# Kernel tuning notes

Measured on AMD Instinct MI355X. Metric: run time of the kernel, lower is better.

## Reference

```python
import jax, jax.numpy as jnp
import numpy as np

B = 2048      # env batch (graphs)
A = 8         # agents per graph (fully connected)
N = B * A     # total nodes
DIN = 192     # raw obs dim
HD = 256      # h_dim (base MLP)
MD = 256      # mem_dim (GRU)
GD = 128      # gnn_dim (per-head GATv2 out, concat=False -> head mean)
H = 4         # GAT heads
NA = 20       # n_actions
ED = 3        # edge_dim


def setup_inputs() -> dict:
    key = jax.random.key(0)
    ks = jax.random.split(key, 16)
    # fully-connected directed graph per group of A agents, no self loops
    s, d = np.meshgrid(np.arange(A), np.arange(A), indexing='ij')
    mask = s != d
    s = s[mask]; d = d[mask]                     # [A*(A-1)]
    off = (np.arange(B) * A)[:, None]
    src = (off + s[None, :]).reshape(-1)
    dst = (off + d[None, :]).reshape(-1)
    edge_index = jnp.asarray(np.stack([src, dst]), dtype=jnp.int32)  # [2, E]
    E = src.shape[0]
    p = lambda k, sh: jax.random.normal(ks[k], sh, jnp.float32) * 0.02
    return {
        'inputs': jax.random.normal(ks[0], (N, DIN), jnp.float32),
        'hidden_states': jax.random.normal(ks[1], (N, MD), jnp.float32) * 0.1,
        'edge_index': edge_index,
        'edge_attr': jax.random.uniform(ks[2], (E, ED), jnp.float32),
        # base MLP (2 layers: Linear+ReLU+LayerNorm)
        'W1': p(3, (DIN, HD)), 'b1': jnp.zeros(HD), 'g1': jnp.ones(HD), 'be1': jnp.zeros(HD),
        'W2': p(4, (HD, HD)),  'b2': jnp.zeros(HD), 'g2': jnp.ones(HD), 'be2': jnp.zeros(HD),
        # GRUCell
        'Wih': p(5, (3 * MD, HD)), 'Whh': p(6, (3 * MD, MD)),
        'bih': jnp.zeros(3 * MD), 'bhh': jnp.zeros(3 * MD),
        # GATv2Conv (edge_dim=3, heads=4, concat=False, residual)
        'Wl': p(7, (MD, H * GD)), 'bl': jnp.zeros(H * GD),
        'Wr': p(8, (MD, H * GD)), 'br': jnp.zeros(H * GD),
        'att': p(9, (H, GD)),
        'We': p(10, (ED, H * GD)),
        'Wres': p(11, (MD, GD)),
        'bg': jnp.zeros(GD),
        # head: LayerNorm + Linear
        'lng': jnp.ones(GD), 'lnb': jnp.zeros(GD),
        'Wout': p(12, (GD, NA)), 'bout': jnp.zeros(NA),
    }


def _ln(x, g, b):
    mu = jnp.mean(x, -1, keepdims=True)
    xc = x - mu
    v = jnp.mean(xc * xc, -1, keepdims=True)
    return xc * jax.lax.rsqrt(v + 1e-5) * g + b


def _fwd(inputs, hidden_states, edge_attr, edge_index,
         W1, b1, g1, be1, W2, b2, g2, be2,
         Wih, Whh, bih, bhh,
         Wl, bl, Wr, br, att, We, Wres, bg,
         lng, lnb, Wout, bout):
    src, dst = edge_index[0], edge_index[1]
    # ---- base MLP encode ----
    x = _ln(jax.nn.relu(inputs @ W1 + b1), g1, be1)
    x = _ln(jax.nn.relu(x @ W2 + b2), g2, be2)          # [N, HD]
    # ---- SimpleConv(aggr='mean', combine_root='self_loop') ----
    s = jax.ops.segment_sum(x[src], dst, num_segments=N) + x
    deg = jax.ops.segment_sum(jnp.ones(src.shape[0], x.dtype), dst, num_segments=N) + 1.0
    x = s / deg[:, None]                                 # [N, HD]
    # ---- GRUCell ----
    gi = x @ Wih.T + bih
    gh = hidden_states @ Whh.T + bhh
    ir, iz, inn = jnp.split(gi, 3, -1)
    hr, hz, hn = jnp.split(gh, 3, -1)
    r = jax.nn.sigmoid(ir + hr)
    z = jax.nn.sigmoid(iz + hz)
    n = jnp.tanh(inn + r * hn)
    h = (1.0 - z) * n + z * hidden_states                # [N, MD]
    # ---- GATv2Conv (add self loops, edge_attr fill='mean') ----
    loop = jnp.arange(N, dtype=src.dtype)
    sf = jnp.concatenate([src, loop])
    df = jnp.concatenate([dst, loop])
    ea = jnp.concatenate([edge_attr, jnp.broadcast_to(edge_attr.mean(0), (N, ED))], 0)
    xl = (h @ Wl + bl).reshape(N, H, GD)
    xr = (h @ Wr + br).reshape(N, H, GD)
    m = xl[sf] + xr[df] + (ea @ We).reshape(-1, H, GD)   # [Ef, H, GD]
    m = jnp.where(m > 0, m, 0.2 * m)                     # leaky_relu(0.2)
    logits = jnp.einsum('ehc,hc->eh', m, att)            # [Ef, H]
    mx = jax.ops.segment_max(logits, df, num_segments=N)
    ex = jnp.exp(logits - mx[df])
    den = jax.ops.segment_sum(ex, df, num_segments=N)
    alpha = ex / (den[df] + 1e-16)                       # segment softmax
    out = jax.ops.segment_sum(xl[sf] * alpha[..., None], df, num_segments=N)
    out = out.mean(1) + h @ Wres + bg                    # head mean + residual + bias
    zg = jax.nn.relu(out)                                # [N, GD]
    # ---- action head ----
    q = _ln(zg, lng, lnb) @ Wout + bout                  # [N, NA]
    return q, h


def reference(inputs, hidden_states, edge_index, edge_attr,
              W1, b1, g1, be1, W2, b2, g2, be2,
              Wih, Whh, bih, bhh,
              Wl, bl, Wr, br, att, We, Wres, bg,
              lng, lnb, Wout, bout):
    return _fwd(inputs, hidden_states, edge_attr, edge_index,
                W1, b1, g1, be1, W2, b2, g2, be2,
                Wih, Whh, bih, bhh,
                Wl, bl, Wr, br, att, We, Wres, bg,
                lng, lnb, Wout, bout)
```

## Files before the change

### kernel.cpp

```cpp
#include <hip/hip_runtime.h>
#include <hip/hip_bf16.h>

constexpr int NB  = 2048;
constexpr int AG  = 8;
constexpr int NN  = NB * AG;
constexpr int DIN = 192;
constexpr int HD  = 256;
constexpr int MD  = 256;
constexpr int GD  = 128;
constexpr int NA  = 20;
constexpr int NE  = NB * AG * (AG - 1);

typedef __attribute__((ext_vector_type(8))) short bfrag8;
typedef __attribute__((ext_vector_type(4))) short sfrag4;
typedef __attribute__((ext_vector_type(4))) float f32x4;

#define MFMA16(a, b, c) __builtin_amdgcn_mfma_f32_16x16x32_bf16((a), (b), (c), 0, 0, 0)

__device__ __forceinline__ float bf2f(__hip_bfloat16 x) { return __bfloat162float(x); }
__device__ __forceinline__ __hip_bfloat16 f2bf(float x) { return __float2bfloat16(x); }
__device__ __forceinline__ short f2bs(float x) {
    __hip_bfloat16 b = __float2bfloat16(x);
    return *reinterpret_cast<short*>(&b);
}
__device__ __forceinline__ bfrag8 ldf(const __hip_bfloat16* p) { return *(const bfrag8*)p; }
__device__ __forceinline__ bfrag8 ldf32(const float* p) {
    const f32x4 a = *(const f32x4*)p;
    const f32x4 b = *(const f32x4*)(p + 4);
    bfrag8 r;
    r[0] = f2bs(a[0]); r[1] = f2bs(a[1]); r[2] = f2bs(a[2]); r[3] = f2bs(a[3]);
    r[4] = f2bs(b[0]); r[5] = f2bs(b[1]); r[6] = f2bs(b[2]); r[7] = f2bs(b[3]);
    return r;
}
__device__ __forceinline__ float sigmf(float x) { return 1.f / (1.f + __expf(-x)); }
__device__ __forceinline__ float blo(unsigned u) { return __uint_as_float(u << 16); }
__device__ __forceinline__ float bhi(unsigned u) { return __uint_as_float(u & 0xffff0000u); }

__global__ __launch_bounds__(256) void k_prep(
    const float* __restrict__ W1, const float* __restrict__ W2,
    const float* __restrict__ Wih, const float* __restrict__ Whh,
    const float* __restrict__ Wl, const float* __restrict__ bl,
    const float* __restrict__ Wr, const float* __restrict__ br,
    const float* __restrict__ Wres, const float* __restrict__ Wout,
    __hip_bfloat16* __restrict__ W1T, __hip_bfloat16* __restrict__ W2T,
    __hip_bfloat16* __restrict__ WihB, __hip_bfloat16* __restrict__ WhhB,
    __hip_bfloat16* __restrict__ WcatT, float* __restrict__ WoutTf,
    float* __restrict__ bcat)
{
    int i = blockIdx.x * 256 + threadIdx.x;
    if (i < 49152) { int o = i / 192, c = i % 192; W1T[i] = f2bf(W1[c * 256 + o]); return; }
    i -= 49152;
    if (i < 65536) { int o = i >> 8, c = i & 255; W2T[i] = f2bf(W2[c * 256 + o]); return; }
    i -= 65536;
    if (i < 196608) { WihB[i] = f2bf(Wih[i]); return; }
    i -= 196608;
    if (i < 196608) { WhhB[i] = f2bf(Whh[i]); return; }
    i -= 196608;
    if (i < 294912) {
        int o = i >> 8, c = i & 255;
        float v;
        if (o < 512)       v = Wl[c * 512 + o];
        else if (o < 1024) v = Wr[c * 512 + (o - 512)];
        else               v = Wres[c * 128 + (o - 1024)];
        WcatT[i] = f2bf(v); return;
    }
    i -= 294912;
    if (i < 2560) { int o = i >> 7, c = i & 127; WoutTf[i] = Wout[c * 20 + o]; return; }
    i -= 2560;
    if (i < 1152) {
        float v = 0.f;
        if (i < 512) v = bl[i]; else if (i < 1024) v = br[i - 512];
        bcat[i] = v;
    }
}

__global__ __launch_bounds__(256) void k_easum1(const float* __restrict__ ea,
                                                float* __restrict__ partials)
{
    __shared__ float sw[4][3];
    const int b = blockIdx.x, tid = threadIdx.x;
    float a0 = 0.f, a1 = 0.f, a2 = 0.f;
#pragma unroll
    for (int k = 0; k < 7; k++) {
        int e = b * 1792 + k * 256 + tid;
        a0 += ea[e * 3 + 0];
        a1 += ea[e * 3 + 1];
        a2 += ea[e * 3 + 2];
    }
#pragma unroll
    for (int off = 1; off < 64; off <<= 1) {
        a0 += __shfl_xor(a0, off); a1 += __shfl_xor(a1, off); a2 += __shfl_xor(a2, off);
    }
    if ((tid & 63) == 0) { sw[tid >> 6][0] = a0; sw[tid >> 6][1] = a1; sw[tid >> 6][2] = a2; }
    __syncthreads();
    if (tid == 0) {
        partials[b * 3 + 0] = sw[0][0] + sw[1][0] + sw[2][0] + sw[3][0];
        partials[b * 3 + 1] = sw[0][1] + sw[1][1] + sw[2][1] + sw[3][1];
        partials[b * 3 + 2] = sw[0][2] + sw[1][2] + sw[2][2] + sw[3][2];
    }
}

__global__ void k_easum2(const float* __restrict__ partials, float* __restrict__ ea_mean)
{
    int t = threadIdx.x;
    if (t < 3) {
        float s = 0.f;
        for (int i = 0; i < 64; i++) s += partials[i * 3 + t];
        ea_mean[t] = s * (1.f / NE);
    }
}

__global__ __launch_bounds__(256) void k_encode(
    const float* __restrict__ in,
    const __hip_bfloat16* __restrict__ W1T,
    const float* __restrict__ b1, const float* __restrict__ g1, const float* __restrict__ be1,
    const __hip_bfloat16* __restrict__ W2T,
    const float* __restrict__ b2, const float* __restrict__ g2, const float* __restrict__ be2,
    __hip_bfloat16* __restrict__ xm)
{
    __shared__ float sf[16][257];
    __shared__ alignas(16) __hip_bfloat16 sb[16][264];
    const int tid = threadIdx.x;
    const int lane = tid & 63, w = tid >> 6;
    const int r = lane & 15, q = lane >> 4;
    const int m0 = blockIdx.x * 16;

    f32x4 acc[4];
#pragma unroll
    for (int i = 0; i < 4; i++) acc[i] = (f32x4){0.f, 0.f, 0.f, 0.f};

    {
        const float* ap = in + (size_t)(m0 + r) * DIN + q * 8;
#pragma unroll
        for (int kb = 0; kb < 6; kb++) {
            bfrag8 af = ldf32(ap + kb * 32);
#pragma unroll
            for (int i = 0; i < 4; i++) {
                int t = w * 4 + i;
                bfrag8 bfv = ldf(W1T + (size_t)(t * 16 + r) * DIN + kb * 32 + q * 8);
                acc[i] = MFMA16(af, bfv, acc[i]);
            }
        }
    }
#pragma unroll
    for (int i = 0; i < 4; i++) {
        int col = (w * 4 + i) * 16 + r;
        float bias = b1[col];
#pragma unroll
        for (int reg = 0; reg < 4; reg++)
            sf[q * 4 + reg][col] = fmaxf(acc[i][reg] + bias, 0.f);
    }
    __syncthreads();
    {
        int rowi = tid >> 4, c16 = tid & 15;
        float vals[16]; float s = 0.f, s2 = 0.f;
#pragma unroll
        for (int j = 0; j < 16; j++) { float v = sf[rowi][c16 + 16 * j]; vals[j] = v; s += v; s2 += v * v; }
#pragma unroll
        for (int off = 1; off < 16; off <<= 1) { s += __shfl_xor(s, off); s2 += __shfl_xor(s2, off); }
        float mean = s * (1.f / HD);
        float var = fmaxf(s2 * (1.f / HD) - mean * mean, 0.f);
        float rs = rsqrtf(var + 1e-5f);
#pragma unroll
        for (int j = 0; j < 16; j++) {
            int col = c16 + 16 * j;
            sb[rowi][col] = f2bf((vals[j] - mean) * rs * g1[col] + be1[col]);
        }
    }
    __syncthreads();

#pragma unroll
    for (int i = 0; i < 4; i++) acc[i] = (f32x4){0.f, 0.f, 0.f, 0.f};
    {
        const __hip_bfloat16* ap = &sb[r][0];
#pragma unroll
        for (int kb = 0; kb < 8; kb++) {
            bfrag8 af = ldf(ap + kb * 32 + q * 8);
#pragma unroll
            for (int i = 0; i < 4; i++) {
                int t = w * 4 + i;
                bfrag8 bfv = ldf(W2T + (size_t)(t * 16 + r) * HD + kb * 32 + q * 8);
                acc[i] = MFMA16(af, bfv, acc[i]);
            }
        }
    }
    __syncthreads();
#pragma unroll
    for (int i = 0; i < 4; i++) {
        int col = (w * 4 + i) * 16 + r;
        float bias = b2[col];
#pragma unroll
        for (int reg = 0; reg < 4; reg++)
            sf[q * 4 + reg][col] = fmaxf(acc[i][reg] + bias, 0.f);
    }
    __syncthreads();
    {
        int rowi = tid >> 4, c16 = tid & 15;
        float vals[16]; float s = 0.f, s2 = 0.f;
#pragma unroll
        for (int j = 0; j < 16; j++) { float v = sf[rowi][c16 + 16 * j]; vals[j] = v; s += v; s2 += v * v; }
#pragma unroll
        for (int off = 1; off < 16; off <<= 1) { s += __shfl_xor(s, off); s2 += __shfl_xor(s2, off); }
        float mean = s * (1.f / HD);
        float var = fmaxf(s2 * (1.f / HD) - mean * mean, 0.f);
        float rs = rsqrtf(var + 1e-5f);
#pragma unroll
        for (int j = 0; j < 16; j++) {
            int col = c16 + 16 * j;
            sb[rowi][col] = f2bf((vals[j] - mean) * rs * g2[col] + be2[col]);
        }
    }
    __syncthreads();
    {
        int col = tid;
        float a0 = 0.f, a1 = 0.f;
#pragma unroll
        for (int i = 0; i < 8; i++) { a0 += bf2f(sb[i][col]); a1 += bf2f(sb[8 + i][col]); }
        xm[(size_t)(2 * blockIdx.x) * HD + col] = f2bf(a0 * 0.125f);
        xm[(size_t)(2 * blockIdx.x + 1) * HD + col] = f2bf(a1 * 0.125f);
    }
}

__global__ __launch_bounds__(256) void k_gi(
    const __hip_bfloat16* __restrict__ xm,
    const __hip_bfloat16* __restrict__ WihB,
    const float* __restrict__ bih,
    float* __restrict__ gi)
{
    const int tid = threadIdx.x;
    const int lane = tid & 63, w = tid >> 6;
    const int r = lane & 15, q = lane >> 4;
    const int m0 = blockIdx.x * 16;

    f32x4 acc[12];
#pragma unroll
    for (int i = 0; i < 12; i++) acc[i] = (f32x4){0.f, 0.f, 0.f, 0.f};
    const __hip_bfloat16* ap = xm + (size_t)(m0 + r) * MD + q * 8;
#pragma unroll
    for (int kb = 0; kb < 8; kb++) {
        bfrag8 af = ldf(ap + kb * 32);
#pragma unroll
        for (int i = 0; i < 12; i++) {
            int t = w * 12 + i;
            bfrag8 bfv = ldf(WihB + (size_t)(t * 16 + r) * MD + kb * 32 + q * 8);
            acc[i] = MFMA16(af, bfv, acc[i]);
        }
    }
#pragma unroll
    for (int i = 0; i < 12; i++) {
        int col = (w * 12 + i) * 16 + r;
        float bias = bih[col];
#pragma unroll
        for (int reg = 0; reg < 4; reg++) {
            int R = m0 + q * 4 + reg;
            gi[(size_t)R * 768 + col] = acc[i][reg] + bias;
        }
    }
}

__global__ __launch_bounds__(256) void k_gru(
    const float* __restrict__ hprev,
    const __hip_bfloat16* __restrict__ WhhB,
    const float* __restrict__ bhh,
    const float* __restrict__ gi,
    float* __restrict__ hout)
{
    const int tid = threadIdx.x;
    const int lane = tid & 63, w = tid >> 6;
    const int r = lane & 15, q = lane >> 4;
    const int m0 = blockIdx.x * 16;

    f32x4 aR[4], aZ[4], aN[4];
#pragma unroll
    for (int i = 0; i < 4; i++) {
        aR[i] = (f32x4){0.f, 0.f, 0.f, 0.f};
        aZ[i] = (f32x4){0.f, 0.f, 0.f, 0.f};
        aN[i] = (f32x4){0.f, 0.f, 0.f, 0.f};
    }
    const float* ap = hprev + (size_t)(m0 + r) * MD + q * 8;
#pragma unroll
    for (int kb = 0; kb < 8; kb++) {
        bfrag8 af = ldf32(ap + kb * 32);
#pragma unroll
        for (int i = 0; i < 4; i++) {
            int ct = w * 4 + i;
            bfrag8 bR = ldf(WhhB + (size_t)(ct * 16 + r) * MD + kb * 32 + q * 8);
            bfrag8 bZ = ldf(WhhB + (size_t)(256 + ct * 16 + r) * MD + kb * 32 + q * 8);
            bfrag8 bN = ldf(WhhB + (size_t)(512 + ct * 16 + r) * MD + kb * 32 + q * 8);
            aR[i] = MFMA16(af, bR, aR[i]);
            aZ[i] = MFMA16(af, bZ, aZ[i]);
            aN[i] = MFMA16(af, bN, aN[i]);
        }
    }
#pragma unroll
    for (int i = 0; i < 4; i++) {
        int c = (w * 4 + i) * 16 + r;
        float bhr = bhh[c], bhz = bhh[256 + c], bhn = bhh[512 + c];
#pragma unroll
        for (int reg = 0; reg < 4; reg++) {
            int R = m0 + q * 4 + reg;
            const float* gir = gi + (size_t)(R >> 3) * 768;
            float rr = sigmf(gir[c] + aR[i][reg] + bhr);
            float zz = sigmf(gir[256 + c] + aZ[i][reg] + bhz);
            float nn = tanhf(gir[512 + c] + rr * (aN[i][reg] + bhn));
            float hp = hprev[(size_t)R * MD + c];
            hout[(size_t)R * MD + c] = (1.f - zz) * nn + zz * hp;
        }
    }
}

__global__ __launch_bounds__(256, 3) void k_gat(
    const float* __restrict__ h,
    const __hip_bfloat16* __restrict__ WcatT,
    const float* __restrict__ bcat,
    const float* __restrict__ ea,
    const float* __restrict__ ea_mean,
    const float* __restrict__ att,
    const float* __restrict__ We,
    const float* __restrict__ bg,
    const float* __restrict__ lng, const float* __restrict__ lnb,
    const float* __restrict__ WoutTf,
    const float* __restrict__ bout,
    float* __restrict__ qout)
{
    __shared__ alignas(16) __hip_bfloat16 sx[16][1160];
    __shared__ float slog[2][4][8][8];
    __shared__ alignas(16) __hip_bfloat16 satt[4][128];
    __shared__ alignas(16) __hip_bfloat16 sWe[3][512];
    __shared__ alignas(16) float szg[16][132];
    const int tid = threadIdx.x;
    const int lane = tid & 63, w = tid >> 6;
    const int r = lane & 15, q = lane >> 4;
    const int m0 = blockIdx.x * 16;

    for (int idx = tid; idx < 512; idx += 256) satt[idx >> 7][idx & 127] = f2bf(att[idx]);
    for (int idx = tid; idx < 1536; idx += 256) sWe[idx / 512][idx % 512] = f2bf(We[idx]);

    float vea[2][3];
    {
        int l = (lane < 56) ? lane : 0;
#pragma unroll
        for (int g = 0; g < 2; g++) {
            const float* ep = ea + (size_t)((blockIdx.x * 2 + g) * 56 + l) * 3;
            vea[g][0] = ep[0]; vea[g][1] = ep[1]; vea[g][2] = ep[2];
        }
    }
    const float em0 = ea_mean[0], em1 = ea_mean[1], em2 = ea_mean[2];

    {
        bfrag8 afr[8];
        const float* ap = h + (size_t)(m0 + r) * MD + q * 8;
#pragma unroll
        for (int kb = 0; kb < 8; kb++) afr[kb] = ldf32(ap + kb * 32);
#pragma unroll
        for (int pass = 0; pass < 2; pass++) {
            f32x4 acc[9];
#pragma unroll
            for (int i = 0; i < 9; i++) acc[i] = (f32x4){0.f, 0.f, 0.f, 0.f};
#pragma unroll
            for (int kb = 0; kb < 8; kb++) {
#pragma unroll
                for (int i = 0; i < 9; i++) {
                    int t = pass * 36 + w * 9 + i;
                    bfrag8 bfv = ldf(WcatT + (size_t)(t * 16 + r) * MD + kb * 32 + q * 8);
                    acc[i] = MFMA16(bfv, afr[kb], acc[i]);
                }
            }
#pragma unroll
            for (int i = 0; i < 9; i++) {
                int fbase = (pass * 36 + w * 9 + i) * 16 + q * 4;
                sfrag4 pk;
#pragma unroll
                for (int reg = 0; reg < 4; reg++)
                    pk[reg] = f2bs(acc[i][reg] + bcat[fbase + reg]);
                *(sfrag4*)&sx[r][fbase] = pk;
            }
        }
    }
    __syncthreads();

    {
        const int li = lane & 31, half = lane >> 5;
#pragma unroll
        for (int t = 0; t < 2; t++) {
            const int combo = w * 2 + t;
            const int gg = combo >> 2, hh = combo & 3;
            uint2 uat = *(const uint2*)&satt[hh][li * 4];
            uint2 u0  = *(const uint2*)&sWe[0][hh * 128 + li * 4];
            uint2 u1  = *(const uint2*)&sWe[1][hh * 128 + li * 4];
            uint2 u2  = *(const uint2*)&sWe[2][hh * 128 + li * 4];
            float at0 = blo(uat.x), at1 = bhi(uat.x), at2 = blo(uat.y), at3 = bhi(uat.y);
            float w00 = blo(u0.x),  w01 = bhi(u0.x),  w02 = blo(u0.y),  w03 = bhi(u0.y);
            float w10 = blo(u1.x),  w11 = bhi(u1.x),  w12 = blo(u1.y),  w13 = bhi(u1.y);
            float w20 = blo(u2.x),  w21 = bhi(u2.x),  w22 = blo(u2.y),  w23 = bhi(u2.y);
            float ve0 = vea[gg][0], ve1 = vea[gg][1], ve2 = vea[gg][2];
            float xv[4][4];
#pragma unroll
            for (int sh = 0; sh < 4; sh++) {
                int sL = sh * 2 + half;
                uint2 uxl = *(const uint2*)&sx[gg * 8 + sL][hh * 128 + li * 4];
                xv[sh][0] = blo(uxl.x); xv[sh][1] = bhi(uxl.x);
                xv[sh][2] = blo(uxl.y); xv[sh][3] = bhi(uxl.y);
            }
            float mylog = 0.f;
#pragma unroll
            for (int d = 0; d < 8; d++) {
                uint2 uxr = *(const uint2*)&sx[gg * 8 + d][512 + hh * 128 + li * 4];
                float xr0 = blo(uxr.x), xr1 = bhi(uxr.x), xr2 = blo(uxr.y), xr3 = bhi(uxr.y);
#pragma unroll
                for (int sh = 0; sh < 4; sh++) {
                    int sL = sh * 2 + half;
                    int el = sL * 7 + d - (d > sL ? 1 : 0);
                    float e0 = __shfl(ve0, el), e1 = __shfl(ve1, el), e2 = __shfl(ve2, el);
                    bool slf = (sL == d);
                    e0 = slf ? em0 : e0; e1 = slf ? em1 : e1; e2 = slf ? em2 : e2;
                    float p, m;
                    m = fmaf(e2, w20, fmaf(e1, w10, fmaf(e0, w00, xv[sh][0]))) + xr0;
                    m = fmaxf(m, 0.2f * m); p = m * at0;
                    m = fmaf(e2, w21, fmaf(e1, w11, fmaf(e0, w01, xv[sh][1]))) + xr1;
                    m = fmaxf(m, 0.2f * m); p = fmaf(m, at1, p);
                    m = fmaf(e2, w22, fmaf(e1, w12, fmaf(e0, w02, xv[sh][2]))) + xr2;
                    m = fmaxf(m, 0.2f * m); p = fmaf(m, at2, p);
                    m = fmaf(e2, w23, fmaf(e1, w13, fmaf(e0, w03, xv[sh][3]))) + xr3;
                    m = fmaxf(m, 0.2f * m); p = fmaf(m, at3, p);
                    p += __shfl_xor(p, 1);  p += __shfl_xor(p, 2);  p += __shfl_xor(p, 4);
                    p += __shfl_xor(p, 8);  p += __shfl_xor(p, 16);
                    float got = __shfl(p, ((lane & 1) << 5) | li);
                    bool want = ((lane >> 3) == d) && (((lane & 7) >> 1) == sh);
                    mylog = want ? got : mylog;
                }
            }
            ((float*)&slog[gg][hh][0][0])[lane] = mylog;
        }
    }
    __syncthreads();

    if (tid < 64) {
        int sg = tid >> 5, sh = (tid >> 3) & 3, d = tid & 7;
        float* L = &slog[sg][sh][d][0];
        float mx = L[0];
#pragma unroll
        for (int s = 1; s < 8; s++) mx = fmaxf(mx, L[s]);
        float ex[8]; float den = 0.f;
#pragma unroll
        for (int s = 0; s < 8; s++) { ex[s] = __expf(L[s] - mx); den += ex[s]; }
        float inv = 1.f / (den + 1e-16f);
#pragma unroll
        for (int s = 0; s < 8; s++) L[s] = ex[s] * inv;
    }
    __syncthreads();

    {
        f32x4 acc0 = (f32x4){0.f, 0.f, 0.f, 0.f};
        f32x4 acc1 = (f32x4){0.f, 0.f, 0.f, 0.f};
        const int ggr = r >> 3, dr = r & 7;
#pragma unroll
        for (int ah = 0; ah < 4; ah++) {
            bfrag8 afA;
#pragma unroll
            for (int j = 0; j < 8; j++) {
                int k = q * 8 + j;
                float v = 0.f;
                if (k < 16) {
                    int ggk = k >> 3, s = k & 7;
                    if (ggk == ggr) v = slog[ggk][ah][dr][s];
                }
                afA[j] = f2bs(v);
            }
#pragma unroll
            for (int j2 = 0; j2 < 2; j2++) {
                int chunk = w * 2 + j2;
                bfrag8 bfB;
#pragma unroll
                for (int j = 0; j < 8; j++) {
                    int k = (q * 8 + j) & 15;
                    bfB[j] = *(const short*)&sx[k][ah * 128 + chunk * 16 + r];
                }
                if (j2 == 0) acc0 = MFMA16(afA, bfB, acc0);
                else         acc1 = MFMA16(afA, bfB, acc1);
            }
        }
#pragma unroll
        for (int j2 = 0; j2 < 2; j2++) {
            f32x4 a = j2 ? acc1 : acc0;
            int c = (w * 2 + j2) * 16 + r;
            float bgc = bg[c];
#pragma unroll
            for (int reg = 0; reg < 4; reg++) {
                int row = q * 4 + reg;
                float o = a[reg] * 0.25f + bf2f(sx[row][1024 + c]) + bgc;
                szg[row][c] = fmaxf(o, 0.f);
            }
        }
    }
    __syncthreads();

    {
        int row = tid >> 4, j = tid & 15;
        float v[8]; float s = 0.f, s2 = 0.f;
#pragma unroll
        for (int cj = 0; cj < 8; cj++) { v[cj] = szg[row][j + 16 * cj]; s += v[cj]; s2 += v[cj] * v[cj]; }
#pragma unroll
        for (int off = 1; off < 16; off <<= 1) { s += __shfl_xor(s, off); s2 += __shfl_xor(s2, off); }
        float mean = s * (1.f / GD);
        float var = fmaxf(s2 * (1.f / GD) - mean * mean, 0.f);
        float rs = rsqrtf(var + 1e-5f);
#pragma unroll
        for (int cj = 0; cj < 8; cj++) {
            int c = j + 16 * cj;
            szg[row][c] = (v[cj] - mean) * rs * lng[c] + lnb[c];
        }
    }
    __syncthreads();

    {
        int row = tid >> 4, j = tid & 15;
        for (int jj = j; jj < NA; jj += 16) {
            float a = bout[jj];
            const float* wo = WoutTf + jj * 128;
#pragma unroll
            for (int c4 = 0; c4 < 32; c4++) {
                f32x4 z = *(const f32x4*)&szg[row][c4 * 4];
                const f32x4 wv = *(const f32x4*)&wo[c4 * 4];
                a = fmaf(z[0], wv[0], a); a = fmaf(z[1], wv[1], a);
                a = fmaf(z[2], wv[2], a); a = fmaf(z[3], wv[3], a);
            }
            qout[(size_t)(m0 + row) * NA + jj] = a;
        }
    }
}

extern "C" void kernel_launch(void* const* d_in, const int* in_sizes, int n_in,
                              void* d_out, int out_size, void* d_ws, size_t ws_size,
                              hipStream_t stream) {
    const float* inp   = (const float*)d_in[0];
    const float* hid   = (const float*)d_in[1];
    const float* eatt  = (const float*)d_in[3];
    const float* W1    = (const float*)d_in[4];
    const float* b1    = (const float*)d_in[5];
    const float* g1    = (const float*)d_in[6];
    const float* be1   = (const float*)d_in[7];
    const float* W2    = (const float*)d_in[8];
    const float* b2    = (const float*)d_in[9];
    const float* g2    = (const float*)d_in[10];
    const float* be2   = (const float*)d_in[11];
    const float* Wih   = (const float*)d_in[12];
    const float* Whh   = (const float*)d_in[13];
    const float* bih   = (const float*)d_in[14];
    const float* bhh   = (const float*)d_in[15];
    const float* Wl    = (const float*)d_in[16];
    const float* bl    = (const float*)d_in[17];
    const float* Wr    = (const float*)d_in[18];
    const float* br    = (const float*)d_in[19];
    const float* att   = (const float*)d_in[20];
    const float* We    = (const float*)d_in[21];
    const float* Wres  = (const float*)d_in[22];
    const float* bg    = (const float*)d_in[23];
    const float* lng   = (const float*)d_in[24];
    const float* lnb   = (const float*)d_in[25];
    const float* Wout  = (const float*)d_in[26];
    const float* bout  = (const float*)d_in[27];

    float* qout = (float*)d_out;
    float* hout = (float*)d_out + (size_t)NN * NA;

    char* ws = (char*)d_ws;
    float*           ea_partials = (float*)ws;
    float*           ea_mean     = (float*)(ws + 1024);
    __hip_bfloat16*  xm    = (__hip_bfloat16*)(ws + 2048);
    float*           gi    = (float*)(ws + 1050624);
    __hip_bfloat16*  W1T   = (__hip_bfloat16*)(ws + 7342080);
    __hip_bfloat16*  W2T   = (__hip_bfloat16*)(ws + 7440384);
    __hip_bfloat16*  WihB  = (__hip_bfloat16*)(ws + 7571456);
    __hip_bfloat16*  WhhB  = (__hip_bfloat16*)(ws + 7964672);
    __hip_bfloat16*  WcatT = (__hip_bfloat16*)(ws + 8357888);
    float*           bcat  = (float*)(ws + 8947712);
    float*           WoutTf= (float*)(ws + 8952320);

    k_easum1<<<64, 256, 0, stream>>>(eatt, ea_partials);
    k_easum2<<<1, 64, 0, stream>>>(ea_partials, ea_mean);
    k_prep<<<3151, 256, 0, stream>>>(W1, W2, Wih, Whh, Wl, bl, Wr, br, Wres, Wout,
                                     W1T, W2T, WihB, WhhB, WcatT, WoutTf, bcat);
    k_encode<<<NN / 16, 256, 0, stream>>>(inp, W1T, b1, g1, be1, W2T, b2, g2, be2, xm);
    k_gi<<<NB / 16, 256, 0, stream>>>(xm, WihB, bih, gi);
    k_gru<<<NN / 16, 256, 0, stream>>>(hid, WhhB, bhh, gi, hout);
    k_gat<<<NN / 16, 256, 0, stream>>>(hout, WcatT, bcat, eatt, ea_mean, att, We, bg,
                                       lng, lnb, WoutTf, bout, qout);
}
```

Measured before the change: 363.6 us.

## Fuse GRU into GAT kernel, merge edge-attr sum into prep, split gi tiles

The GRU cell is computed inside the GAT kernel, and the new hidden state is kept in shared memory as bf16 for the GAT projection. This removes one kernel launch and a global re-read of h. The edge-attr partial sums move into extra blocks of the prep kernel, and each GAT block finishes the mean itself, which drops two launches. k_gi now launches twice as many blocks, each computing half the output tiles, to raise parallelism. The cost is more registers and shared memory in the fused kernel, which may reduce occupancy.

```diff
diff --git a/kernel.cpp b/kernel.cpp
--- a/kernel.cpp
+++ b/kernel.cpp
@@ -42,12 +42,38 @@
     const float* __restrict__ Wl, const float* __restrict__ bl,
     const float* __restrict__ Wr, const float* __restrict__ br,
     const float* __restrict__ Wres, const float* __restrict__ Wout,
+    const float* __restrict__ ea,
     __hip_bfloat16* __restrict__ W1T, __hip_bfloat16* __restrict__ W2T,
     __hip_bfloat16* __restrict__ WihB, __hip_bfloat16* __restrict__ WhhB,
     __hip_bfloat16* __restrict__ WcatT, float* __restrict__ WoutTf,
-    float* __restrict__ bcat)
+    float* __restrict__ bcat, float* __restrict__ ea_partials)
 {
-    int i = blockIdx.x * 256 + threadIdx.x;
+    __shared__ float sw[4][3];
+    const int tid = threadIdx.x;
+    if (blockIdx.x >= 3151) {
+        const int b = blockIdx.x - 3151;
+        float a0 = 0.f, a1 = 0.f, a2 = 0.f;
+#pragma unroll
+        for (int k = 0; k < 7; k++) {
+            int e = b * 1792 + k * 256 + tid;
+            a0 += ea[e * 3 + 0];
+            a1 += ea[e * 3 + 1];
+            a2 += ea[e * 3 + 2];
+        }
+#pragma unroll
+        for (int off = 1; off < 64; off <<= 1) {
+            a0 += __shfl_xor(a0, off); a1 += __shfl_xor(a1, off); a2 += __shfl_xor(a2, off);
+        }
+        if ((tid & 63) == 0) { sw[tid >> 6][0] = a0; sw[tid >> 6][1] = a1; sw[tid >> 6][2] = a2; }
+        __syncthreads();
+        if (tid == 0) {
+            ea_partials[b * 3 + 0] = sw[0][0] + sw[1][0] + sw[2][0] + sw[3][0];
+            ea_partials[b * 3 + 1] = sw[0][1] + sw[1][1] + sw[2][1] + sw[3][1];
+            ea_partials[b * 3 + 2] = sw[0][2] + sw[1][2] + sw[2][2] + sw[3][2];
+        }
+        return;
+    }
+    int i = blockIdx.x * 256 + tid;
     if (i < 49152) { int o = i / 192, c = i % 192; W1T[i] = f2bf(W1[c * 256 + o]); return; }
     i -= 49152;
     if (i < 65536) { int o = i >> 8, c = i & 255; W2T[i] = f2bf(W2[c * 256 + o]); return; }
@@ -74,42 +100,6 @@
     }
 }
 
-__global__ __launch_bounds__(256) void k_easum1(const float* __restrict__ ea,
-                                                float* __restrict__ partials)
-{
-    __shared__ float sw[4][3];
-    const int b = blockIdx.x, tid = threadIdx.x;
-    float a0 = 0.f, a1 = 0.f, a2 = 0.f;
-#pragma unroll
-    for (int k = 0; k < 7; k++) {
-        int e = b * 1792 + k * 256 + tid;
-        a0 += ea[e * 3 + 0];
-        a1 += ea[e * 3 + 1];
-        a2 += ea[e * 3 + 2];
-    }
-#pragma unroll
-    for (int off = 1; off < 64; off <<= 1) {
-        a0 += __shfl_xor(a0, off); a1 += __shfl_xor(a1, off); a2 += __shfl_xor(a2, off);
-    }
-    if ((tid & 63) == 0) { sw[tid >> 6][0] = a0; sw[tid >> 6][1] = a1; sw[tid >> 6][2] = a2; }
-    __syncthreads();
-    if (tid == 0) {
-        partials[b * 3 + 0] = sw[0][0] + sw[1][0] + sw[2][0] + sw[3][0];
-        partials[b * 3 + 1] = sw[0][1] + sw[1][1] + sw[2][1] + sw[3][1];
-        partials[b * 3 + 2] = sw[0][2] + sw[1][2] + sw[2][2] + sw[3][2];
-    }
-}
-
-__global__ void k_easum2(const float* __restrict__ partials, float* __restrict__ ea_mean)
-{
-    int t = threadIdx.x;
-    if (t < 3) {
-        float s = 0.f;
-        for (int i = 0; i < 64; i++) s += partials[i * 3 + t];
-        ea_mean[t] = s * (1.f / NE);
-    }
-}
-
 __global__ __launch_bounds__(256) void k_encode(
     const float* __restrict__ in,
     const __hip_bfloat16* __restrict__ W1T,
@@ -230,25 +220,26 @@
     const int tid = threadIdx.x;
     const int lane = tid & 63, w = tid >> 6;
     const int r = lane & 15, q = lane >> 4;
-    const int m0 = blockIdx.x * 16;
-
-    f32x4 acc[12];
-#pragma unroll
-    for (int i = 0; i < 12; i++) acc[i] = (f32x4){0.f, 0.f, 0.f, 0.f};
+    const int m0 = (blockIdx.x >> 1) * 16;
+    const int t0 = (blockIdx.x & 1) * 24;
+
+    f32x4 acc[6];
+#pragma unroll
+    for (int i = 0; i < 6; i++) acc[i] = (f32x4){0.f, 0.f, 0.f, 0.f};
     const __hip_bfloat16* ap = xm + (size_t)(m0 + r) * MD + q * 8;
 #pragma unroll
     for (int kb = 0; kb < 8; kb++) {
         bfrag8 af = ldf(ap + kb * 32);
 #pragma unroll
-        for (int i = 0; i < 12; i++) {
-            int t = w * 12 + i;
+        for (int i = 0; i < 6; i++) {
+            int t = t0 + w * 6 + i;
             bfrag8 bfv = ldf(WihB + (size_t)(t * 16 + r) * MD + kb * 32 + q * 8);
             acc[i] = MFMA16(af, bfv, acc[i]);
         }
     }
 #pragma unroll
-    for (int i = 0; i < 12; i++) {
-        int col = (w * 12 + i) * 16 + r;
+    for (int i = 0; i < 6; i++) {
+        int col = (t0 + w * 6 + i) * 16 + r;
         float bias = bih[col];
 #pragma unroll
         for (int reg = 0; reg < 4; reg++) {
@@ -258,76 +249,32 @@
     }
 }
 
-__global__ __launch_bounds__(256) void k_gru(
+__global__ __launch_bounds__(256, 3) void k_gatgru(
     const float* __restrict__ hprev,
     const __hip_bfloat16* __restrict__ WhhB,
     const float* __restrict__ bhh,
     const float* __restrict__ gi,
-    float* __restrict__ hout)
-{
-    const int tid = threadIdx.x;
-    const int lane = tid & 63, w = tid >> 6;
-    const int r = lane & 15, q = lane >> 4;
-    const int m0 = blockIdx.x * 16;
-
-    f32x4 aR[4], aZ[4], aN[4];
-#pragma unroll
-    for (int i = 0; i < 4; i++) {
-        aR[i] = (f32x4){0.f, 0.f, 0.f, 0.f};
-        aZ[i] = (f32x4){0.f, 0.f, 0.f, 0.f};
-        aN[i] = (f32x4){0.f, 0.f, 0.f, 0.f};
-    }
-    const float* ap = hprev + (size_t)(m0 + r) * MD + q * 8;
-#pragma unroll
-    for (int kb = 0; kb < 8; kb++) {
-        bfrag8 af = ldf32(ap + kb * 32);
-#pragma unroll
-        for (int i = 0; i < 4; i++) {
-            int ct = w * 4 + i;
-            bfrag8 bR = ldf(WhhB + (size_t)(ct * 16 + r) * MD + kb * 32 + q * 8);
-            bfrag8 bZ = ldf(WhhB + (size_t)(256 + ct * 16 + r) * MD + kb * 32 + q * 8);
-            bfrag8 bN = ldf(WhhB + (size_t)(512 + ct * 16 + r) * MD + kb * 32 + q * 8);
-            aR[i] = MFMA16(af, bR, aR[i]);
-            aZ[i] = MFMA16(af, bZ, aZ[i]);
-            aN[i] = MFMA16(af, bN, aN[i]);
-        }
-    }
-#pragma unroll
-    for (int i = 0; i < 4; i++) {
-        int c = (w * 4 + i) * 16 + r;
-        float bhr = bhh[c], bhz = bhh[256 + c], bhn = bhh[512 + c];
-#pragma unroll
-        for (int reg = 0; reg < 4; reg++) {
-            int R = m0 + q * 4 + reg;
-            const float* gir = gi + (size_t)(R >> 3) * 768;
-            float rr = sigmf(gir[c] + aR[i][reg] + bhr);
-            float zz = sigmf(gir[256 + c] + aZ[i][reg] + bhz);
-            float nn = tanhf(gir[512 + c] + rr * (aN[i][reg] + bhn));
-            float hp = hprev[(size_t)R * MD + c];
-            hout[(size_t)R * MD + c] = (1.f - zz) * nn + zz * hp;
-        }
-    }
-}
-
-__global__ __launch_bounds__(256, 3) void k_gat(
-    const float* __restrict__ h,
     const __hip_bfloat16* __restrict__ WcatT,
     const float* __restrict__ bcat,
     const float* __restrict__ ea,
-    const float* __restrict__ ea_mean,
+    const float* __restrict__ ea_partials,
     const float* __restrict__ att,
     const float* __restrict__ We,
     const float* __restrict__ bg,
     const float* __restrict__ lng, const float* __restrict__ lnb,
     const float* __restrict__ WoutTf,
     const float* __restrict__ bout,
+    float* __restrict__ hout,
     float* __restrict__ qout)
 {
     __shared__ alignas(16) __hip_bfloat16 sx[16][1160];
+    __shared__ alignas(16) unsigned char u_shszg[16 * 272 * 2];
     __shared__ float slog[2][4][8][8];
     __shared__ alignas(16) __hip_bfloat16 satt[4][128];
     __shared__ alignas(16) __hip_bfloat16 sWe[3][512];
-    __shared__ alignas(16) float szg[16][132];
+    __shared__ float smean[4];
+    auto sh  = (__hip_bfloat16(*)[272])u_shszg;
+    auto szg = (float(*)[136])u_shszg;
     const int tid = threadIdx.x;
     const int lane = tid & 63, w = tid >> 6;
     const int r = lane & 15, q = lane >> 4;
@@ -335,6 +282,11 @@
 
     for (int idx = tid; idx < 512; idx += 256) satt[idx >> 7][idx & 127] = f2bf(att[idx]);
     for (int idx = tid; idx < 1536; idx += 256) sWe[idx / 512][idx % 512] = f2bf(We[idx]);
+    if (tid < 3) {
+        float s = 0.f;
+        for (int i = 0; i < 64; i++) s += ea_partials[i * 3 + tid];
+        smean[tid] = s * (1.f / NE);
+    }
 
     float vea[2][3];
     {
@@ -345,13 +297,54 @@
             vea[g][0] = ep[0]; vea[g][1] = ep[1]; vea[g][2] = ep[2];
         }
     }
-    const float em0 = ea_mean[0], em1 = ea_mean[1], em2 = ea_mean[2];
+
+    {
+        f32x4 aR[4], aZ[4], aN[4];
+#pragma unroll
+        for (int i = 0; i < 4; i++) {
+            aR[i] = (f32x4){0.f, 0.f, 0.f, 0.f};
+            aZ[i] = (f32x4){0.f, 0.f, 0.f, 0.f};
+            aN[i] = (f32x4){0.f, 0.f, 0.f, 0.f};
+        }
+        const float* ap = hprev + (size_t)(m0 + r) * MD + q * 8;
+#pragma unroll
+        for (int kb = 0; kb < 8; kb++) {
+            bfrag8 af = ldf32(ap + kb * 32);
+#pragma unroll
+            for (int i = 0; i < 4; i++) {
+                int ct = w * 4 + i;
+                bfrag8 bR = ldf(WhhB + (size_t)(ct * 16 + r) * MD + kb * 32 + q * 8);
+                bfrag8 bZ = ldf(WhhB + (size_t)(256 + ct * 16 + r) * MD + kb * 32 + q * 8);
+                bfrag8 bN = ldf(WhhB + (size_t)(512 + ct * 16 + r) * MD + kb * 32 + q * 8);
+                aR[i] = MFMA16(af, bR, aR[i]);
+                aZ[i] = MFMA16(af, bZ, aZ[i]);
+                aN[i] = MFMA16(af, bN, aN[i]);
+            }
+        }
+#pragma unroll
+        for (int i = 0; i < 4; i++) {
+            int c = (w * 4 + i) * 16 + r;
+            float bhr = bhh[c], bhz = bhh[256 + c], bhn = bhh[512 + c];
+#pragma unroll
+            for (int reg = 0; reg < 4; reg++) {
+                int R = m0 + q * 4 + reg;
+                const float* gir = gi + (size_t)(R >> 3) * 768;
+                float rr = sigmf(gir[c] + aR[i][reg] + bhr);
+                float zz = sigmf(gir[256 + c] + aZ[i][reg] + bhz);
+                float nn = tanhf(gir[512 + c] + rr * (aN[i][reg] + bhn));
+                float hp = hprev[(size_t)R * MD + c];
+                float hv = (1.f - zz) * nn + zz * hp;
+                hout[(size_t)R * MD + c] = hv;
+                sh[q * 4 + reg][c] = f2bf(hv);
+            }
+        }
+    }
+    __syncthreads();
 
     {
         bfrag8 afr[8];
-        const float* ap = h + (size_t)(m0 + r) * MD + q * 8;
-#pragma unroll
-        for (int kb = 0; kb < 8; kb++) afr[kb] = ldf32(ap + kb * 32);
+#pragma unroll
+        for (int kb = 0; kb < 8; kb++) afr[kb] = ldf(&sh[r][kb * 32 + q * 8]);
 #pragma unroll
         for (int pass = 0; pass < 2; pass++) {
             f32x4 acc[9];
@@ -378,6 +371,7 @@
         }
     }
     __syncthreads();
+    const float em0 = smean[0], em1 = smean[1], em2 = smean[2];
 
     {
         const int li = lane & 31, half = lane >> 5;
@@ -396,11 +390,11 @@
             float ve0 = vea[gg][0], ve1 = vea[gg][1], ve2 = vea[gg][2];
             float xv[4][4];
 #pragma unroll
-            for (int sh = 0; sh < 4; sh++) {
-                int sL = sh * 2 + half;
+            for (int sh2 = 0; sh2 < 4; sh2++) {
+                int sL = sh2 * 2 + half;
                 uint2 uxl = *(const uint2*)&sx[gg * 8 + sL][hh * 128 + li * 4];
-                xv[sh][0] = blo(uxl.x); xv[sh][1] = bhi(uxl.x);
-                xv[sh][2] = blo(uxl.y); xv[sh][3] = bhi(uxl.y);
+                xv[sh2][0] = blo(uxl.x); xv[sh2][1] = bhi(uxl.x);
+                xv[sh2][2] = blo(uxl.y); xv[sh2][3] = bhi(uxl.y);
             }
             float mylog = 0.f;
 #pragma unroll
@@ -408,25 +402,25 @@
                 uint2 uxr = *(const uint2*)&sx[gg * 8 + d][512 + hh * 128 + li * 4];
                 float xr0 = blo(uxr.x), xr1 = bhi(uxr.x), xr2 = blo(uxr.y), xr3 = bhi(uxr.y);
 #pragma unroll
-                for (int sh = 0; sh < 4; sh++) {
-                    int sL = sh * 2 + half;
+                for (int sh2 = 0; sh2 < 4; sh2++) {
+                    int sL = sh2 * 2 + half;
                     int el = sL * 7 + d - (d > sL ? 1 : 0);
                     float e0 = __shfl(ve0, el), e1 = __shfl(ve1, el), e2 = __shfl(ve2, el);
                     bool slf = (sL == d);
                     e0 = slf ? em0 : e0; e1 = slf ? em1 : e1; e2 = slf ? em2 : e2;
                     float p, m;
-                    m = fmaf(e2, w20, fmaf(e1, w10, fmaf(e0, w00, xv[sh][0]))) + xr0;
+                    m = fmaf(e2, w20, fmaf(e1, w10, fmaf(e0, w00, xv[sh2][0]))) + xr0;
                     m = fmaxf(m, 0.2f * m); p = m * at0;
-                    m = fmaf(e2, w21, fmaf(e1, w11, fmaf(e0, w01, xv[sh][1]))) + xr1;
+                    m = fmaf(e2, w21, fmaf(e1, w11, fmaf(e0, w01, xv[sh2][1]))) + xr1;
                     m = fmaxf(m, 0.2f * m); p = fmaf(m, at1, p);
-                    m = fmaf(e2, w22, fmaf(e1, w12, fmaf(e0, w02, xv[sh][2]))) + xr2;
+                    m = fmaf(e2, w22, fmaf(e1, w12, fmaf(e0, w02, xv[sh2][2]))) + xr2;
                     m = fmaxf(m, 0.2f * m); p = fmaf(m, at2, p);
-                    m = fmaf(e2, w23, fmaf(e1, w13, fmaf(e0, w03, xv[sh][3]))) + xr3;
+                    m = fmaf(e2, w23, fmaf(e1, w13, fmaf(e0, w03, xv[sh2][3]))) + xr3;
                     m = fmaxf(m, 0.2f * m); p = fmaf(m, at3, p);
                     p += __shfl_xor(p, 1);  p += __shfl_xor(p, 2);  p += __shfl_xor(p, 4);
                     p += __shfl_xor(p, 8);  p += __shfl_xor(p, 16);
                     float got = __shfl(p, ((lane & 1) << 5) | li);
-                    bool want = ((lane >> 3) == d) && (((lane & 7) >> 1) == sh);
+                    bool want = ((lane >> 3) == d) && (((lane & 7) >> 1) == sh2);
                     mylog = want ? got : mylog;
                 }
             }
@@ -436,8 +430,8 @@
     __syncthreads();
 
     if (tid < 64) {
-        int sg = tid >> 5, sh = (tid >> 3) & 3, d = tid & 7;
-        float* L = &slog[sg][sh][d][0];
+        int sg = tid >> 5, sh2 = (tid >> 3) & 3, d = tid & 7;
+        float* L = &slog[sg][sh2][d][0];
         float mx = L[0];
 #pragma unroll
         for (int s = 1; s < 8; s++) mx = fmaxf(mx, L[s]);
@@ -566,7 +560,6 @@
 
     char* ws = (char*)d_ws;
     float*           ea_partials = (float*)ws;
-    float*           ea_mean     = (float*)(ws + 1024);
     __hip_bfloat16*  xm    = (__hip_bfloat16*)(ws + 2048);
     float*           gi    = (float*)(ws + 1050624);
     __hip_bfloat16*  W1T   = (__hip_bfloat16*)(ws + 7342080);
@@ -577,13 +570,11 @@
     float*           bcat  = (float*)(ws + 8947712);
     float*           WoutTf= (float*)(ws + 8952320);
 
-    k_easum1<<<64, 256, 0, stream>>>(eatt, ea_partials);
-    k_easum2<<<1, 64, 0, stream>>>(ea_partials, ea_mean);
-    k_prep<<<3151, 256, 0, stream>>>(W1, W2, Wih, Whh, Wl, bl, Wr, br, Wres, Wout,
-                                     W1T, W2T, WihB, WhhB, WcatT, WoutTf, bcat);
+    k_prep<<<3215, 256, 0, stream>>>(W1, W2, Wih, Whh, Wl, bl, Wr, br, Wres, Wout, eatt,
+                                     W1T, W2T, WihB, WhhB, WcatT, WoutTf, bcat, ea_partials);
     k_encode<<<NN / 16, 256, 0, stream>>>(inp, W1T, b1, g1, be1, W2T, b2, g2, be2, xm);
-    k_gi<<<NB / 16, 256, 0, stream>>>(xm, WihB, bih, gi);
-    k_gru<<<NN / 16, 256, 0, stream>>>(hid, WhhB, bhh, gi, hout);
-    k_gat<<<NN / 16, 256, 0, stream>>>(hout, WcatT, bcat, eatt, ea_mean, att, We, bg,
-                                       lng, lnb, WoutTf, bout, qout);
-}
+    k_gi<<<256, 256, 0, stream>>>(xm, WihB, bih, gi);
+    k_gatgru<<<NN / 16, 256, 0, stream>>>(hid, WhhB, bhh, gi, WcatT, bcat, eatt,
+                                          ea_partials, att, We, bg, lng, lnb,
+                                          WoutTf, bout, hout, qout);
+}
```

Result: no change. 359.5 us (-1.1%).
